# Kernel tuning notes

Measured on AMD Instinct MI355X. Metric: run time of the kernel, lower is better.

## Reference

```python
import jax, jax.numpy as jnp
import numpy as np

B, NX, NR, D, H = 8, 512, 512, 256, 256


def setup_inputs() -> dict:
    key = jax.random.key(0)
    ks = jax.random.split(key, 8)
    s = 1.0 / np.sqrt(D)
    sh = 1.0 / np.sqrt(H)
    return {
        "X": jax.random.normal(ks[0], (B, NX, D), dtype=jnp.float32),
        "ref": jax.random.normal(ks[1], (B, NR, D), dtype=jnp.float32),
        "W_X": jax.random.normal(ks[2], (H, D), dtype=jnp.float32) * s,
        "b_X": jax.random.normal(ks[3], (H,), dtype=jnp.float32) * s,
        "W_ref": jax.random.normal(ks[4], (H, D), dtype=jnp.float32) * s,
        "b_ref": jax.random.normal(ks[5], (H,), dtype=jnp.float32) * s,
        "v_w": jax.random.normal(ks[6], (1, H), dtype=jnp.float32) * sh,
        "v_b": jax.random.normal(ks[7], (1,), dtype=jnp.float32) * sh,
    }


def reference(X, ref, W_X, b_X, W_ref, b_ref, v_w, v_b):
    # linear projections: [B, nX, H], [B, nR, H]
    hX = jnp.einsum('bxd,hd->bxh', X, W_X) + b_X
    hR = jnp.einsum('brd,hd->brh', ref, W_ref) + b_ref
    # additive (Bahdanau) scores: [B, nX, nR]
    t = jnp.tanh(hX[:, :, None, :] + hR[:, None, :, :])
    out = jnp.einsum('bxrh,h->bxr', t, v_w[0]) + v_b[0]
    # softmax over the n_X axis (dim=1 in torch)
    attn = jax.nn.softmax(out, axis=1)
    # weighted sum of X per ref position: [B, nR, D]
    weighted_X = jnp.einsum('bxe,bxr->bre', X, attn)
    return weighted_X
```

## Files before the change

kernel.cpp:

```cpp
#include <hip/hip_runtime.h>
#include <math.h>

#define CB 8
#define CNX 512
#define CNR 512
#define CD 256
#define CH 256

__device__ __forceinline__ float fast_rcp(float x) {
#if __has_builtin(__builtin_amdgcn_rcpf)
  return __builtin_amdgcn_rcpf(x);
#else
  return 1.0f / x;
#endif
}
__device__ __forceinline__ float fast_exp2(float x) {
#if __has_builtin(__builtin_amdgcn_exp2f)
  return __builtin_amdgcn_exp2f(x);
#else
  return exp2f(x);
#endif
}

__global__ __launch_bounds__(256) void proj_fused(
    const float* __restrict__ A0, const float* __restrict__ A1,
    const float* __restrict__ W0, const float* __restrict__ W1,
    const float* __restrict__ bias0, const float* __restrict__ bias1,
    float* __restrict__ E0, float* __restrict__ E1) {
  __shared__ float As[16][68];
  __shared__ float Ws[16][68];
  const int K = CD;
  int z = blockIdx.z;
  const float* A = z ? A1 : A0;
  const float* W = z ? W1 : W0;
  const float* bias = z ? bias1 : bias0;
  float* ET = z ? E1 : E0;
  int m0 = blockIdx.x * 64, n0 = blockIdx.y * 64;
  int tid = threadIdx.x;
  int tx = tid & 15, ty = tid >> 4;
  int lrow = tid >> 2, lc4 = tid & 3;
  float acc[4][4] = {};
  const float* pA = A + (size_t)(m0 + lrow) * K + lc4 * 4;
  const float* pW = W + (size_t)(n0 + lrow) * K + lc4 * 4;
  float4 av = *(const float4*)(pA);
  float4 wv = *(const float4*)(pW);
  for (int kt = 0; kt < K; kt += 16) {
    __syncthreads();
    As[lc4 * 4 + 0][lrow] = av.x;
    As[lc4 * 4 + 1][lrow] = av.y;
    As[lc4 * 4 + 2][lrow] = av.z;
    As[lc4 * 4 + 3][lrow] = av.w;
    Ws[lc4 * 4 + 0][lrow] = wv.x;
    Ws[lc4 * 4 + 1][lrow] = wv.y;
    Ws[lc4 * 4 + 2][lrow] = wv.z;
    Ws[lc4 * 4 + 3][lrow] = wv.w;
    __syncthreads();
    if (kt + 16 < K) {
      av = *(const float4*)(pA + kt + 16);
      wv = *(const float4*)(pW + kt + 16);
    }
#pragma unroll
    for (int k = 0; k < 16; k++) {
      float4 a4 = *(const float4*)&As[k][ty * 4];
      float4 w4 = *(const float4*)&Ws[k][tx * 4];
      float am[4] = {a4.x, a4.y, a4.z, a4.w};
      float wm[4] = {w4.x, w4.y, w4.z, w4.w};
#pragma unroll
      for (int i = 0; i < 4; i++)
#pragma unroll
        for (int j = 0; j < 4; j++)
          acc[i][j] = fmaf(am[i], wm[j], acc[i][j]);
    }
  }
  const float K2L = 2.8853900817779268f;
  float4 bv = *(const float4*)(bias + n0 + tx * 4);
  float bm[4] = {bv.x, bv.y, bv.z, bv.w};
  int b = m0 >> 9;
  int xbase = (m0 & 511) + ty * 4;
#pragma unroll
  for (int j = 0; j < 4; j++) {
    int h = n0 + tx * 4 + j;
    float4 o = {fast_exp2(K2L * (acc[0][j] + bm[j])),
                fast_exp2(K2L * (acc[1][j] + bm[j])),
                fast_exp2(K2L * (acc[2][j] + bm[j])),
                fast_exp2(K2L * (acc[3][j] + bm[j]))};
    *(float4*)(ET + ((size_t)b * CH + h) * CNX + xbase) = o;
  }
}

#define HCH 32
__global__ __launch_bounds__(256) void scores_kernel(
    const float* __restrict__ exT, const float* __restrict__ erT,
    const float* __restrict__ v_w, float* __restrict__ scT) {
  __shared__ float xs[HCH][64];
  __shared__ float rs[HCH][64];
  __shared__ float vsh[CH];
  int b = blockIdx.z;
  int x0 = blockIdx.x * 64, r0 = blockIdx.y * 64;
  int tid = threadIdx.x;
  int tx = tid & 15, ty = tid >> 4;
  vsh[tid] = v_w[tid];
  int sr = ty, sc = tx * 4;
  const float* pX = exT + (size_t)b * CH * CNX + x0 + sc;
  const float* pR = erT + (size_t)b * CH * CNR + r0 + sc;
  float4 xa0 = *(const float4*)(pX + (size_t)sr * CNX);
  float4 xa1 = *(const float4*)(pX + (size_t)(sr + 16) * CNX);
  float4 ra0 = *(const float4*)(pR + (size_t)sr * CNR);
  float4 ra1 = *(const float4*)(pR + (size_t)(sr + 16) * CNR);
  float acc[4][4] = {};
  for (int hc = 0; hc < CH; hc += HCH) {
    __syncthreads();
    *(float4*)&xs[sr][sc] = xa0;
    *(float4*)&xs[sr + 16][sc] = xa1;
    *(float4*)&rs[sr][sc] = ra0;
    *(float4*)&rs[sr + 16][sc] = ra1;
    __syncthreads();
    if (hc + HCH < CH) {
      xa0 = *(const float4*)(pX + (size_t)(hc + HCH + sr) * CNX);
      xa1 = *(const float4*)(pX + (size_t)(hc + HCH + sr + 16) * CNX);
      ra0 = *(const float4*)(pR + (size_t)(hc + HCH + sr) * CNR);
      ra1 = *(const float4*)(pR + (size_t)(hc + HCH + sr + 16) * CNR);
    }
#pragma unroll 2
    for (int hq = 0; hq < HCH / 4; hq++) {
      int h0 = hq * 4;
      float4 vv = *(const float4*)&vsh[hc + h0];
      float4 xv0 = *(const float4*)&xs[h0 + 0][tx * 4];
      float4 xv1 = *(const float4*)&xs[h0 + 1][tx * 4];
      float4 xv2 = *(const float4*)&xs[h0 + 2][tx * 4];
      float4 xv3 = *(const float4*)&xs[h0 + 3][tx * 4];
      float4 rv0 = *(const float4*)&rs[h0 + 0][ty * 4];
      float4 rv1 = *(const float4*)&rs[h0 + 1][ty * 4];
      float4 rv2 = *(const float4*)&rs[h0 + 2][ty * 4];
      float4 rv3 = *(const float4*)&rs[h0 + 3][ty * 4];
      float xm0[4] = {xv0.x, xv0.y, xv0.z, xv0.w};
      float xm1[4] = {xv1.x, xv1.y, xv1.z, xv1.w};
      float xm2[4] = {xv2.x, xv2.y, xv2.z, xv2.w};
      float xm3[4] = {xv3.x, xv3.y, xv3.z, xv3.w};
      float rm0[4] = {rv0.x, rv0.y, rv0.z, rv0.w};
      float rm1[4] = {rv1.x, rv1.y, rv1.z, rv1.w};
      float rm2[4] = {rv2.x, rv2.y, rv2.z, rv2.w};
      float rm3[4] = {rv3.x, rv3.y, rv3.z, rv3.w};
#pragma unroll
      for (int i = 0; i < 4; i++)
#pragma unroll
        for (int j = 0; j < 4; j++) {
          float a = fmaf(rm0[i], xm0[j], 1.0f);
          float bb = fmaf(rm1[i], xm1[j], 1.0f);
          float c = fmaf(rm2[i], xm2[j], 1.0f);
          float d = fmaf(rm3[i], xm3[j], 1.0f);
          float q12 = a * bb, q34 = c * d;
          float p12 = fmaf(vv.y, a, vv.x * bb);
          float p34 = fmaf(vv.w, c, vv.z * d);
          float num = fmaf(p34, q12, p12 * q34);
          acc[i][j] = fmaf(num, fast_rcp(q12 * q34), acc[i][j]);
        }
    }
  }
  float* pO = scT + ((size_t)b * CNR + r0 + ty * 4) * CNX + x0 + tx * 4;
#pragma unroll
  for (int i = 0; i < 4; i++) {
    float4 o = {-2.0f * acc[i][0], -2.0f * acc[i][1],
                -2.0f * acc[i][2], -2.0f * acc[i][3]};
    *(float4*)(pO + (size_t)i * CNX) = o;
  }
}

__global__ __launch_bounds__(256) void wsum_fused(
    const float* __restrict__ scT, const float* __restrict__ X,
    float* __restrict__ out) {
  __shared__ float As[32][68];
  __shared__ float Bs[32][68];
  __shared__ float dn[64];
  const float L2E = 1.4426950408889634f;
  int b = blockIdx.z;
  int r0 = blockIdx.x * 64, d0 = blockIdx.y * 64;
  int tid = threadIdx.x;
  int tx = tid & 15, ty = tid >> 4;
  int ar = tid >> 2, ak = (tid & 3) * 4;
  int br = tid >> 4, bc = (tid & 15) * 4;
  const float* pS = scT + ((size_t)b * CNR + r0 + ar) * CNX + ak;
  const float* pB = X + (size_t)b * CNX * CD + d0 + bc;
  float acc[4][4] = {};
  float dsum = 0.0f;
  float4 s0 = *(const float4*)(pS);
  float4 s1 = *(const float4*)(pS + 16);
  float4 b0 = *(const float4*)(pB + (size_t)br * CD);
  float4 b1 = *(const float4*)(pB + (size_t)(br + 16) * CD);
  for (int kt = 0; kt < CNX; kt += 32) {
    float4 e0 = {fast_exp2(s0.x * L2E), fast_exp2(s0.y * L2E),
                 fast_exp2(s0.z * L2E), fast_exp2(s0.w * L2E)};
    float4 e1 = {fast_exp2(s1.x * L2E), fast_exp2(s1.y * L2E),
                 fast_exp2(s1.z * L2E), fast_exp2(s1.w * L2E)};
    dsum += ((e0.x + e0.y) + (e0.z + e0.w)) + ((e1.x + e1.y) + (e1.z + e1.w));
    __syncthreads();
    As[ak + 0][ar] = e0.x;
    As[ak + 1][ar] = e0.y;
    As[ak + 2][ar] = e0.z;
    As[ak + 3][ar] = e0.w;
    As[ak + 16][ar] = e1.x;
    As[ak + 17][ar] = e1.y;
    As[ak + 18][ar] = e1.z;
    As[ak + 19][ar] = e1.w;
    *(float4*)&Bs[br][bc] = b0;
    *(float4*)&Bs[br + 16][bc] = b1;
    __syncthreads();
    if (kt + 32 < CNX) {
      s0 = *(const float4*)(pS + kt + 32);
      s1 = *(const float4*)(pS + kt + 48);
      b0 = *(const float4*)(pB + (size_t)(kt + 32 + br) * CD);
      b1 = *(const float4*)(pB + (size_t)(kt + 32 + br + 16) * CD);
    }
#pragma unroll 8
    for (int k = 0; k < 32; k++) {
      float4 a4 = *(const float4*)&As[k][ty * 4];
      float4 b4 = *(const float4*)&Bs[k][tx * 4];
      float am[4] = {a4.x, a4.y, a4.z, a4.w};
      float bm[4] = {b4.x, b4.y, b4.z, b4.w};
#pragma unroll
      for (int i = 0; i < 4; i++)
#pragma unroll
        for (int j = 0; j < 4; j++)
          acc[i][j] = fmaf(am[i], bm[j], acc[i][j]);
    }
  }
  dsum += __shfl_xor(dsum, 1, 64);
  dsum += __shfl_xor(dsum, 2, 64);
  if ((tid & 3) == 0) dn[ar] = dsum;
  __syncthreads();
  float invm[4] = {fast_rcp(dn[ty * 4 + 0]), fast_rcp(dn[ty * 4 + 1]),
                   fast_rcp(dn[ty * 4 + 2]), fast_rcp(dn[ty * 4 + 3])};
  float* pO = out + ((size_t)b * CNR + r0 + ty * 4) * CD + d0 + tx * 4;
#pragma unroll
  for (int i = 0; i < 4; i++) {
    float4 o = {acc[i][0] * invm[i], acc[i][1] * invm[i],
                acc[i][2] * invm[i], acc[i][3] * invm[i]};
    *(float4*)(pO + (size_t)i * CD) = o;
  }
}

extern "C" void kernel_launch(void* const* d_in, const int* in_sizes, int n_in,
                              void* d_out, int out_size, void* d_ws, size_t ws_size,
                              hipStream_t stream) {
  const float* X     = (const float*)d_in[0];
  const float* ref   = (const float*)d_in[1];
  const float* W_X   = (const float*)d_in[2];
  const float* b_X   = (const float*)d_in[3];
  const float* W_ref = (const float*)d_in[4];
  const float* b_ref = (const float*)d_in[5];
  const float* v_w   = (const float*)d_in[6];
  float* out = (float*)d_out;
  float* ws  = (float*)d_ws;

  float* exT = ws;
  float* erT = ws + 1048576;
  float* scT = ws + 2097152;

  proj_fused<<<dim3(64, 4, 2), 256, 0, stream>>>(X, ref, W_X, W_ref, b_X, b_ref, exT, erT);
  scores_kernel<<<dim3(8, 8, 8), 256, 0, stream>>>(exT, erT, v_w, scT);
  wsum_fused<<<dim3(8, 4, 8), 256, 0, stream>>>(scT, X, out);
}
```

Baseline: 155.8 us.

## Split reduction dimension across two thread groups in scores and wsum kernels

Both the scores and weighted-sum kernels now launch 512 threads per block, split into two 256-thread groups. Each group processes alternating 32-wide chunks of the reduction dimension (H for scores, NX for wsum) in its own shared-memory tiles, and the partial accumulators are merged through shared memory at the end. The aim is to double the waves per block and improve latency hiding, since the grids are small (512 and 256 blocks). The cost is higher shared-memory use per block, an extra merge pass, and extra block-wide synchronisation.

Result: faster. 152.5 us (-2.1%).

```diff
diff --git a/kernel.cpp b/kernel.cpp
--- a/kernel.cpp
+++ b/kernel.cpp
@@ -88,51 +88,54 @@
   }
 }
 
-#define HCH 32
-__global__ __launch_bounds__(256) void scores_kernel(
+__global__ __launch_bounds__(512) void scores_kernel(
     const float* __restrict__ exT, const float* __restrict__ erT,
     const float* __restrict__ v_w, float* __restrict__ scT) {
-  __shared__ float xs[HCH][64];
-  __shared__ float rs[HCH][64];
-  __shared__ float vsh[CH];
+  __shared__ float smem[4 * 2048 + 256];
   int b = blockIdx.z;
   int x0 = blockIdx.x * 64, r0 = blockIdx.y * 64;
   int tid = threadIdx.x;
-  int tx = tid & 15, ty = tid >> 4;
-  vsh[tid] = v_w[tid];
-  int sr = ty, sc = tx * 4;
+  int g = tid >> 8;
+  int t = tid & 255;
+  float* xs = smem + g * 4096;
+  float* rs = xs + 2048;
+  float* vsh = smem + 8192;
+  if (tid < 256) vsh[tid] = v_w[tid];
+  int tx = t & 15, ty = t >> 4;
+  int sr = t >> 4, sc = (t & 15) * 4;
   const float* pX = exT + (size_t)b * CH * CNX + x0 + sc;
   const float* pR = erT + (size_t)b * CH * CNR + r0 + sc;
-  float4 xa0 = *(const float4*)(pX + (size_t)sr * CNX);
-  float4 xa1 = *(const float4*)(pX + (size_t)(sr + 16) * CNX);
-  float4 ra0 = *(const float4*)(pR + (size_t)sr * CNR);
-  float4 ra1 = *(const float4*)(pR + (size_t)(sr + 16) * CNR);
+  int hb = g * 32;
+  float4 xa0 = *(const float4*)(pX + (size_t)(hb + sr) * CNX);
+  float4 xa1 = *(const float4*)(pX + (size_t)(hb + sr + 16) * CNX);
+  float4 ra0 = *(const float4*)(pR + (size_t)(hb + sr) * CNR);
+  float4 ra1 = *(const float4*)(pR + (size_t)(hb + sr + 16) * CNR);
   float acc[4][4] = {};
-  for (int hc = 0; hc < CH; hc += HCH) {
-    __syncthreads();
-    *(float4*)&xs[sr][sc] = xa0;
-    *(float4*)&xs[sr + 16][sc] = xa1;
-    *(float4*)&rs[sr][sc] = ra0;
-    *(float4*)&rs[sr + 16][sc] = ra1;
-    __syncthreads();
-    if (hc + HCH < CH) {
-      xa0 = *(const float4*)(pX + (size_t)(hc + HCH + sr) * CNX);
-      xa1 = *(const float4*)(pX + (size_t)(hc + HCH + sr + 16) * CNX);
-      ra0 = *(const float4*)(pR + (size_t)(hc + HCH + sr) * CNR);
-      ra1 = *(const float4*)(pR + (size_t)(hc + HCH + sr + 16) * CNR);
+  for (int hc = hb; hc < CH; hc += 64) {
+    __syncthreads();
+    *(float4*)&xs[sr * 64 + sc] = xa0;
+    *(float4*)&xs[(sr + 16) * 64 + sc] = xa1;
+    *(float4*)&rs[sr * 64 + sc] = ra0;
+    *(float4*)&rs[(sr + 16) * 64 + sc] = ra1;
+    __syncthreads();
+    if (hc + 64 < CH) {
+      xa0 = *(const float4*)(pX + (size_t)(hc + 64 + sr) * CNX);
+      xa1 = *(const float4*)(pX + (size_t)(hc + 64 + sr + 16) * CNX);
+      ra0 = *(const float4*)(pR + (size_t)(hc + 64 + sr) * CNR);
+      ra1 = *(const float4*)(pR + (size_t)(hc + 64 + sr + 16) * CNR);
     }
 #pragma unroll 2
-    for (int hq = 0; hq < HCH / 4; hq++) {
+    for (int hq = 0; hq < 8; hq++) {
       int h0 = hq * 4;
       float4 vv = *(const float4*)&vsh[hc + h0];
-      float4 xv0 = *(const float4*)&xs[h0 + 0][tx * 4];
-      float4 xv1 = *(const float4*)&xs[h0 + 1][tx * 4];
-      float4 xv2 = *(const float4*)&xs[h0 + 2][tx * 4];
-      float4 xv3 = *(const float4*)&xs[h0 + 3][tx * 4];
-      float4 rv0 = *(const float4*)&rs[h0 + 0][ty * 4];
-      float4 rv1 = *(const float4*)&rs[h0 + 1][ty * 4];
-      float4 rv2 = *(const float4*)&rs[h0 + 2][ty * 4];
-      float4 rv3 = *(const float4*)&rs[h0 + 3][ty * 4];
+      float4 xv0 = *(const float4*)&xs[(h0 + 0) * 64 + tx * 4];
+      float4 xv1 = *(const float4*)&xs[(h0 + 1) * 64 + tx * 4];
+      float4 xv2 = *(const float4*)&xs[(h0 + 2) * 64 + tx * 4];
+      float4 xv3 = *(const float4*)&xs[(h0 + 3) * 64 + tx * 4];
+      float4 rv0 = *(const float4*)&rs[(h0 + 0) * 64 + ty * 4];
+      float4 rv1 = *(const float4*)&rs[(h0 + 1) * 64 + ty * 4];
+      float4 rv2 = *(const float4*)&rs[(h0 + 2) * 64 + ty * 4];
+      float4 rv3 = *(const float4*)&rs[(h0 + 3) * 64 + ty * 4];
       float xm0[4] = {xv0.x, xv0.y, xv0.z, xv0.w};
       float xm1[4] = {xv1.x, xv1.y, xv1.z, xv1.w};
       float xm2[4] = {xv2.x, xv2.y, xv2.z, xv2.w};
@@ -157,64 +160,82 @@
         }
     }
   }
-  float* pO = scT + ((size_t)b * CNR + r0 + ty * 4) * CNX + x0 + tx * 4;
-#pragma unroll
-  for (int i = 0; i < 4; i++) {
-    float4 o = {-2.0f * acc[i][0], -2.0f * acc[i][1],
-                -2.0f * acc[i][2], -2.0f * acc[i][3]};
-    *(float4*)(pO + (size_t)i * CNX) = o;
-  }
-}
-
-__global__ __launch_bounds__(256) void wsum_fused(
+  __syncthreads();
+  float* mg = smem;
+  if (g == 1) {
+#pragma unroll
+    for (int i = 0; i < 4; i++)
+#pragma unroll
+      for (int j = 0; j < 4; j++)
+        mg[t + 256 * (i * 4 + j)] = acc[i][j];
+  }
+  __syncthreads();
+  if (g == 0) {
+    float* pO = scT + ((size_t)b * CNR + r0 + ty * 4) * CNX + x0 + tx * 4;
+#pragma unroll
+    for (int i = 0; i < 4; i++) {
+      float4 o = {-2.0f * (acc[i][0] + mg[t + 256 * (i * 4 + 0)]),
+                  -2.0f * (acc[i][1] + mg[t + 256 * (i * 4 + 1)]),
+                  -2.0f * (acc[i][2] + mg[t + 256 * (i * 4 + 2)]),
+                  -2.0f * (acc[i][3] + mg[t + 256 * (i * 4 + 3)])};
+      *(float4*)(pO + (size_t)i * CNX) = o;
+    }
+  }
+}
+
+__global__ __launch_bounds__(512) void wsum_fused(
     const float* __restrict__ scT, const float* __restrict__ X,
     float* __restrict__ out) {
-  __shared__ float As[32][68];
-  __shared__ float Bs[32][68];
-  __shared__ float dn[64];
+  __shared__ float smem[4 * 2176 + 128];
   const float L2E = 1.4426950408889634f;
   int b = blockIdx.z;
   int r0 = blockIdx.x * 64, d0 = blockIdx.y * 64;
   int tid = threadIdx.x;
-  int tx = tid & 15, ty = tid >> 4;
-  int ar = tid >> 2, ak = (tid & 3) * 4;
-  int br = tid >> 4, bc = (tid & 15) * 4;
+  int g = tid >> 8;
+  int t = tid & 255;
+  float* As = smem + g * 4352;
+  float* Bs = As + 2176;
+  float* dnn = smem + 8704;
+  int tx = t & 15, ty = t >> 4;
+  int ar = t >> 2, ak = (t & 3) * 4;
+  int br = t >> 4, bc = (t & 15) * 4;
+  int kb = g * 32;
   const float* pS = scT + ((size_t)b * CNR + r0 + ar) * CNX + ak;
   const float* pB = X + (size_t)b * CNX * CD + d0 + bc;
   float acc[4][4] = {};
   float dsum = 0.0f;
-  float4 s0 = *(const float4*)(pS);
-  float4 s1 = *(const float4*)(pS + 16);
-  float4 b0 = *(const float4*)(pB + (size_t)br * CD);
-  float4 b1 = *(const float4*)(pB + (size_t)(br + 16) * CD);
-  for (int kt = 0; kt < CNX; kt += 32) {
+  float4 s0 = *(const float4*)(pS + kb);
+  float4 s1 = *(const float4*)(pS + kb + 16);
+  float4 b0 = *(const float4*)(pB + (size_t)(kb + br) * CD);
+  float4 b1 = *(const float4*)(pB + (size_t)(kb + br + 16) * CD);
+  for (int kt = kb; kt < CNX; kt += 64) {
     float4 e0 = {fast_exp2(s0.x * L2E), fast_exp2(s0.y * L2E),
                  fast_exp2(s0.z * L2E), fast_exp2(s0.w * L2E)};
     float4 e1 = {fast_exp2(s1.x * L2E), fast_exp2(s1.y * L2E),
                  fast_exp2(s1.z * L2E), fast_exp2(s1.w * L2E)};
     dsum += ((e0.x + e0.y) + (e0.z + e0.w)) + ((e1.x + e1.y) + (e1.z + e1.w));
     __syncthreads();
-    As[ak + 0][ar] = e0.x;
-    As[ak + 1][ar] = e0.y;
-    As[ak + 2][ar] = e0.z;
-    As[ak + 3][ar] = e0.w;
-    As[ak + 16][ar] = e1.x;
-    As[ak + 17][ar] = e1.y;
-    As[ak + 18][ar] = e1.z;
-    As[ak + 19][ar] = e1.w;
-    *(float4*)&Bs[br][bc] = b0;
-    *(float4*)&Bs[br + 16][bc] = b1;
-    __syncthreads();
-    if (kt + 32 < CNX) {
-      s0 = *(const float4*)(pS + kt + 32);
-      s1 = *(const float4*)(pS + kt + 48);
-      b0 = *(const float4*)(pB + (size_t)(kt + 32 + br) * CD);
-      b1 = *(const float4*)(pB + (size_t)(kt + 32 + br + 16) * CD);
+    As[(ak + 0) * 68 + ar] = e0.x;
+    As[(ak + 1) * 68 + ar] = e0.y;
+    As[(ak + 2) * 68 + ar] = e0.z;
+    As[(ak + 3) * 68 + ar] = e0.w;
+    As[(ak + 16) * 68 + ar] = e1.x;
+    As[(ak + 17) * 68 + ar] = e1.y;
+    As[(ak + 18) * 68 + ar] = e1.z;
+    As[(ak + 19) * 68 + ar] = e1.w;
+    *(float4*)&Bs[br * 68 + bc] = b0;
+    *(float4*)&Bs[(br + 16) * 68 + bc] = b1;
+    __syncthreads();
+    if (kt + 64 < CNX) {
+      s0 = *(const float4*)(pS + kt + 64);
+      s1 = *(const float4*)(pS + kt + 80);
+      b0 = *(const float4*)(pB + (size_t)(kt + 64 + br) * CD);
+      b1 = *(const float4*)(pB + (size_t)(kt + 64 + br + 16) * CD);
     }
 #pragma unroll 8
     for (int k = 0; k < 32; k++) {
-      float4 a4 = *(const float4*)&As[k][ty * 4];
-      float4 b4 = *(const float4*)&Bs[k][tx * 4];
+      float4 a4 = *(const float4*)&As[k * 68 + ty * 4];
+      float4 b4 = *(const float4*)&Bs[k * 68 + tx * 4];
       float am[4] = {a4.x, a4.y, a4.z, a4.w};
       float bm[4] = {b4.x, b4.y, b4.z, b4.w};
 #pragma unroll
@@ -226,16 +247,32 @@
   }
   dsum += __shfl_xor(dsum, 1, 64);
   dsum += __shfl_xor(dsum, 2, 64);
-  if ((tid & 3) == 0) dn[ar] = dsum;
-  __syncthreads();
-  float invm[4] = {fast_rcp(dn[ty * 4 + 0]), fast_rcp(dn[ty * 4 + 1]),
-                   fast_rcp(dn[ty * 4 + 2]), fast_rcp(dn[ty * 4 + 3])};
-  float* pO = out + ((size_t)b * CNR + r0 + ty * 4) * CD + d0 + tx * 4;
-#pragma unroll
-  for (int i = 0; i < 4; i++) {
-    float4 o = {acc[i][0] * invm[i], acc[i][1] * invm[i],
-                acc[i][2] * invm[i], acc[i][3] * invm[i]};
-    *(float4*)(pO + (size_t)i * CD) = o;
+  if ((t & 3) == 0) dnn[g * 64 + ar] = dsum;
+  __syncthreads();
+  float* mg = smem;
+  if (g == 1) {
+#pragma unroll
+    for (int i = 0; i < 4; i++)
+#pragma unroll
+      for (int j = 0; j < 4; j++)
+        mg[t + 256 * (i * 4 + j)] = acc[i][j];
+  }
+  __syncthreads();
+  if (g == 0) {
+    float invm[4];
+#pragma unroll
+    for (int i = 0; i < 4; i++)
+      invm[i] = fast_rcp(dnn[ty * 4 + i] + dnn[64 + ty * 4 + i]);
+    float* pO = out + ((size_t)b * CNR + r0 + ty * 4) * CD + d0 + tx * 4;
+#pragma unroll
+    for (int i = 0; i < 4; i++) {
+      float4 o = {
+          (acc[i][0] + mg[t + 256 * (i * 4 + 0)]) * invm[i],
+          (acc[i][1] + mg[t + 256 * (i * 4 + 1)]) * invm[i],
+          (acc[i][2] + mg[t + 256 * (i * 4 + 2)]) * invm[i],
+          (acc[i][3] + mg[t + 256 * (i * 4 + 3)]) * invm[i]};
+      *(float4*)(pO + (size_t)i * CD) = o;
+    }
   }
 }
 
@@ -257,6 +294,6 @@
   float* scT = ws + 2097152;
 
   proj_fused<<<dim3(64, 4, 2), 256, 0, stream>>>(X, ref, W_X, W_ref, b_X, b_ref, exT, erT);
-  scores_kernel<<<dim3(8, 8, 8), 256, 0, stream>>>(exT, erT, v_w, scT);
-  wsum_fused<<<dim3(8, 4, 8), 256, 0, stream>>>(scT, X, out);
-}
+  scores_kernel<<<dim3(8, 8, 8), 512, 0, stream>>>(exT, erT, v_w, scT);
+  wsum_fused<<<dim3(8, 4, 8), 512, 0, stream>>>(scT, X, out);
+}
```
